# Kernel tuning notes

Hardware: AMD Instinct MI355X
Metric: run time of the kernel (lower is better)

Reference implementation:

```python
import jax, jax.numpy as jnp
import numpy as np

KH = KW = 3
STRIDE = 1
ITERATIONS = 2
EPS = 1e-7


def _squash(s):
    # squash along last axis (capsule dim)
    sn = jnp.sum(s * s, axis=-1, keepdims=True)
    return (sn / (1.0 + sn)) * s / jnp.sqrt(sn + EPS)


def setup_inputs() -> dict:
    key = jax.random.key(0)
    k1, k2 = jax.random.split(key)
    x = jax.random.normal(k1, (4, 14, 14, 32, 8), dtype=jnp.float32)
    # W: [1,1,1,filters_out, caps_per_patch=3*3*32, dims_out=16, dims_in=8], stddev=0.1 init
    W = 0.1 * jax.random.normal(k2, (1, 1, 1, 32, 288, 16, 8), dtype=jnp.float32)
    return {"x": x, "W": W}


def reference(x, W):
    B, H, Wd, Fin, Din = x.shape
    Ho = (H - KH) // STRIDE + 1
    Wo = (Wd - KW) // STRIDE + 1
    # Patch extraction, channel order (kh, kw, Fin) to match tf.image.extract_patches
    patches = jnp.stack(
        [x[:, i:i + Ho * STRIDE:STRIDE, j:j + Wo * STRIDE:STRIDE]
         for i in range(KH) for j in range(KW)],
        axis=3,
    )  # [B,Ho,Wo,KH*KW,Fin,Din]
    patches = patches.reshape(B, Ho, Wo, KH * KW * Fin, Din)  # [B,Ho,Wo,C,Di]

    Wm = W[0, 0, 0]  # [F, C, Do, Di]
    F, C, Do, _ = Wm.shape
    # predictions[b,h,w,f,c,o] = sum_i W[f,c,o,i] * patches[b,h,w,c,i]
    preds = jnp.einsum('fcoi,bhwci->bhwfco', Wm, patches)

    logits = jnp.zeros((B, Ho, Wo, F, C), dtype=preds.dtype)
    outputs = jnp.zeros((B, Ho, Wo, F, Do), dtype=preds.dtype)
    for _ in range(ITERATIONS):
        # agreement = predictions^T @ outputs over the dims_out axis
        agreement = jnp.einsum('bhwfco,bhwfo->bhwfc', preds, outputs)
        logits = logits + agreement
        # NOTE: original code softmaxes over axis=3 (the filters_out axis)
        cc = jax.nn.softmax(logits, axis=3)  # [B,Ho,Wo,F,C]
        centroids = jnp.sum(cc[..., None] * preds, axis=4)  # [B,Ho,Wo,F,Do]
        outputs = _squash(centroids)
    return outputs
```

## Files before the change

### kernel.cpp

```cpp
#include <hip/hip_runtime.h>

#define NB   4
#define H_IN 14
#define W_IN 14
#define FIN  32
#define DI   8
#define F    32
#define C    288
#define DO   16
#define HO   12
#define WO   12
#define NPOS (NB*HO*WO)
#define EPS  1e-7f

#define CH   16
#define CC   (C/CH)
#define GP   2
#define GRID2 ((CH*NPOS/GP)/4)

#define KTOT  (C*DI)
#define KHALF 1152
#define KPADH 1156

#define W2H_BYTES  ((size_t)F*C*DO*DI*2)
#define WH_BYTES   ((size_t)F*C*DO*DI*2)
#define PH_BYTES   ((size_t)NPOS*KTOT*2)
#define PART_BYTES ((size_t)CH*NPOS*F*DO*4)
#define OUT1P_BYTES ((size_t)2*NPOS*F*DO*4)

#define CVT_W   576
#define CVT_PH  648
#define CVT_GRID (CVT_W + CVT_PH)

typedef _Float16 h2 __attribute__((ext_vector_type(2)));
typedef _Float16 h8v __attribute__((ext_vector_type(8)));
typedef float    f4v __attribute__((ext_vector_type(4)));

__device__ __forceinline__ unsigned int pack2(float a, float b) {
    h2 v; v.x = (_Float16)a; v.y = (_Float16)b;
    return __builtin_bit_cast(unsigned int, v);
}

__device__ __forceinline__ float dot8h(const uint4 w, const uint4 v, float acc) {
#if __has_builtin(__builtin_amdgcn_fdot2)
    acc = __builtin_amdgcn_fdot2(__builtin_bit_cast(h2, w.x), __builtin_bit_cast(h2, v.x), acc, false);
    acc = __builtin_amdgcn_fdot2(__builtin_bit_cast(h2, w.y), __builtin_bit_cast(h2, v.y), acc, false);
    acc = __builtin_amdgcn_fdot2(__builtin_bit_cast(h2, w.z), __builtin_bit_cast(h2, v.z), acc, false);
    acc = __builtin_amdgcn_fdot2(__builtin_bit_cast(h2, w.w), __builtin_bit_cast(h2, v.w), acc, false);
#else
    const h2 w0 = __builtin_bit_cast(h2, w.x), v0 = __builtin_bit_cast(h2, v.x);
    const h2 w1 = __builtin_bit_cast(h2, w.y), v1 = __builtin_bit_cast(h2, v.y);
    const h2 w2 = __builtin_bit_cast(h2, w.z), v2 = __builtin_bit_cast(h2, v.z);
    const h2 w3 = __builtin_bit_cast(h2, w.w), v3 = __builtin_bit_cast(h2, v.w);
    acc += (float)w0.x*(float)v0.x + (float)w0.y*(float)v0.y
         + (float)w1.x*(float)v1.x + (float)w1.y*(float)v1.y
         + (float)w2.x*(float)v2.x + (float)w2.y*(float)v2.y
         + (float)w3.x*(float)v3.x + (float)w3.y*(float)v3.y;
#endif
    return acc;
}

__device__ __forceinline__ int xbase_of(int pos) {
    const int b = pos/(HO*WO), rem = pos%(HO*WO), ho = rem/WO, wo = rem%WO;
    return ((b*H_IN + ho)*W_IN + wo)*FIN*DI;
}

__device__ __forceinline__ int coff_of(int c) {
    const int slab = c >> 5, fin = c & 31;
    const int kh = slab/3, kw = slab%3;
    return (kh*W_IN + kw)*FIN*DI + fin*DI;
}

__global__ __launch_bounds__(256) void kernConv(const float* __restrict__ Wt,
                                                const float* __restrict__ x,
                                                unsigned short* __restrict__ W2h,
                                                unsigned short* __restrict__ Wh,
                                                unsigned short* __restrict__ Ph) {
    const int b = blockIdx.x;
    if (b < CVT_W) {
        const int idx = b*256 + threadIdx.x;
        const float* src = Wt + (size_t)idx*8;
        const float4 a = *(const float4*)src;
        const float4 bb = *(const float4*)(src + 4);
        uint4 r;
        r.x = pack2(a.x, a.y);   r.y = pack2(a.z, a.w);
        r.z = pack2(bb.x, bb.y); r.w = pack2(bb.z, bb.w);
        ((uint4*)Wh)[idx] = r;
        const int o = idx & 15;
        const int c = (idx >> 4) % C;
        const int f = idx / (C*DO);
        ((uint4*)W2h)[(size_t)(c*DO + o)*F + f] = r;
    } else {
        const int pc = (b - CVT_W)*256 + threadIdx.x;
        const int pos = pc / C, c = pc % C;
        const float* src = x + xbase_of(pos) + coff_of(c);
        const float4 a = *(const float4*)src;
        const float4 bb = *(const float4*)(src + 4);
        uint4 r;
        r.x = pack2(a.x, a.y);   r.y = pack2(a.z, a.w);
        r.z = pack2(bb.x, bb.y); r.w = pack2(bb.z, bb.w);
        ((uint4*)Ph)[pc] = r;
    }
}

__global__ __launch_bounds__(256) void kernM1(const unsigned short* __restrict__ Ph,
                                              const unsigned short* __restrict__ Wh,
                                              float* __restrict__ out1p)
{
    __shared__ unsigned short As[16][KPADH];

    const int tid  = threadIdx.x;
    const int lane = tid & 63;
    const int wv   = tid >> 6;
    const int ks   = blockIdx.x & 1;
    const int fg   = (blockIdx.x >> 1) & 7;
    const int pt   = blockIdx.x >> 4;
    const int f    = wv*8 + fg;
    const int pos0 = pt*16;
    const int n    = lane & 15, q = lane >> 4;

    #pragma unroll
    for (int r = 0; r < 9; ++r) {
        const int linear = r*256 + tid;
        const int row = linear / 144, col = linear % 144;
        const uint4 v = *(const uint4*)(Ph + (size_t)(pos0 + row)*KTOT + ks*KHALF + col*8);
        *(uint4*)&As[row][col*8] = v;
    }
    __syncthreads();

    const unsigned short* pa = &As[n][q*8];
    const unsigned short* pb = Wh + ((size_t)(f*C + ks*144 + q)*DO + n)*DI;

    f4v acc0 = {0.f,0.f,0.f,0.f}, acc1 = {0.f,0.f,0.f,0.f};
    #pragma unroll 4
    for (int s = 0; s < 36; s += 2) {
        const h8v a0 = *(const h8v*)(pa + s*32);
        const h8v b0 = *(const h8v*)(pb + (size_t)s*4*DO*DI);
        const h8v a1 = *(const h8v*)(pa + (s+1)*32);
        const h8v b1 = *(const h8v*)(pb + (size_t)(s+1)*4*DO*DI);
        acc0 = __builtin_amdgcn_mfma_f32_16x16x32_f16(a0, b0, acc0, 0, 0, 0);
        acc1 = __builtin_amdgcn_mfma_f32_16x16x32_f16(a1, b1, acc1, 0, 0, 0);
    }

    #pragma unroll
    for (int r = 0; r < 4; ++r) {
        out1p[((size_t)ks*NPOS + pos0 + q*4 + r)*512 + f*DO + n] = acc0[r] + acc1[r];
    }
}

__global__ __launch_bounds__(256) void kern2w(const unsigned short* __restrict__ Ph,
                                              const unsigned short* __restrict__ W2h,
                                              const float* __restrict__ out1p,
                                              float* __restrict__ part2)
{
    const int tid  = threadIdx.x;
    const int lane = tid & 63;
    const int wv   = tid >> 6;
    const int f    = lane & 31;
    const int og   = lane >> 5;
    const int o0   = og*8;

    const int ch   = blockIdx.x & (CH-1);
    const int gq   = blockIdx.x >> 4;
    const int grp  = __builtin_amdgcn_readfirstlane(gq*4 + wv);
    const int pos0 = grp*GP;

    const int c0 = ch*CC;
    const uint4* W2h4 = (const uint4*)W2h;

    float u[8][GP];
    #pragma unroll
    for (int p = 0; p < GP; ++p) {
        const float* up0 = out1p + (size_t)(pos0 + p)*512 + f*DO + o0;
        const float* up1 = up0 + (size_t)NPOS*512;
        const float4 a0 = *(const float4*)up0;
        const float4 b0 = *(const float4*)(up0 + 4);
        const float4 a1 = *(const float4*)up1;
        const float4 b1 = *(const float4*)(up1 + 4);
        float ur[8];
        ur[0]=(a0.x+a1.x)*(1.f/32.f); ur[1]=(a0.y+a1.y)*(1.f/32.f);
        ur[2]=(a0.z+a1.z)*(1.f/32.f); ur[3]=(a0.w+a1.w)*(1.f/32.f);
        ur[4]=(b0.x+b1.x)*(1.f/32.f); ur[5]=(b0.y+b1.y)*(1.f/32.f);
        ur[6]=(b0.z+b1.z)*(1.f/32.f); ur[7]=(b0.w+b1.w)*(1.f/32.f);
        float sq = 0.f;
        #pragma unroll
        for (int k = 0; k < 8; ++k) sq += ur[k]*ur[k];
        sq += __shfl_xor(sq, 32);
        const float sc = (sq/(1.f + sq)) * rsqrtf(sq + EPS);
        #pragma unroll
        for (int k = 0; k < 8; ++k) u[k][p] = ur[k]*sc;
    }

    float acc[8][GP];
    #pragma unroll
    for (int k = 0; k < 8; ++k)
        #pragma unroll
        for (int p = 0; p < GP; ++p) acc[k][p] = 0.f;

    #pragma unroll 1
    for (int cl = 0; cl < CC; ++cl) {
        const int c = c0 + cl;

        uint4 xv[GP];
        #pragma unroll
        for (int p = 0; p < GP; ++p)
            xv[p] = *(const uint4*)(Ph + (size_t)(pos0 + p)*KTOT + c*DI);

        float pred[8][GP];
        #pragma unroll
        for (int k = 0; k < 8; ++k) {
            const uint4 w = W2h4[(size_t)(c*DO + o0 + k)*F + f];
            #pragma unroll
            for (int p = 0; p < GP; ++p) pred[k][p] = dot8h(w, xv[p], 0.f);
        }

        #pragma unroll
        for (int p = 0; p < GP; ++p) {
            float ap = 0.f;
            #pragma unroll
            for (int k = 0; k < 8; ++k) ap += pred[k][p]*u[k][p];
            ap += __shfl_xor(ap, 32);

            const float e = __expf(ap);
            float s = e;
            s += __shfl_xor(s, 1);
            s += __shfl_xor(s, 2);
            s += __shfl_xor(s, 4);
            s += __shfl_xor(s, 8);
            s += __shfl_xor(s, 16);
            const float cc = e / s;

            #pragma unroll
            for (int k = 0; k < 8; ++k) acc[k][p] += cc*pred[k][p];
        }
    }

    #pragma unroll
    for (int p = 0; p < GP; ++p) {
        float* dst = part2 + ((size_t)(ch*NPOS + pos0 + p)*F + f)*DO + o0;
        float4 s0, s1;
        s0.x=acc[0][p]; s0.y=acc[1][p]; s0.z=acc[2][p]; s0.w=acc[3][p];
        s1.x=acc[4][p]; s1.y=acc[5][p]; s1.z=acc[6][p]; s1.w=acc[7][p];
        *(float4*)dst = s0;
        *(float4*)(dst + 4) = s1;
    }
}

__global__ __launch_bounds__(256) void kern3(const float* __restrict__ part2,
                                             float* __restrict__ out)
{
    __shared__ float4 red[128];

    const int tid  = threadIdx.x;
    const int pos  = blockIdx.x;
    const int half = tid >> 7;
    const int slot = tid & 127;
    const int f = slot >> 2, q = slot & 3;

    float ax=0.f, ay=0.f, az=0.f, aw=0.f;
    #pragma unroll
    for (int k = 0; k < CH/2; ++k) {
        const int kk = half*(CH/2) + k;
        const float4 v = *(const float4*)(part2 + ((size_t)(kk*NPOS + pos)*F + f)*DO + q*4);
        ax += v.x; ay += v.y; az += v.z; aw += v.w;
    }
    if (half) { float4 r; r.x=ax; r.y=ay; r.z=az; r.w=aw; red[slot] = r; }
    __syncthreads();
    if (!half) {
        const float4 o = red[slot];
        ax += o.x; ay += o.y; az += o.z; aw += o.w;

        float sq = ax*ax + ay*ay + az*az + aw*aw;
        sq += __shfl_xor(sq, 1);
        sq += __shfl_xor(sq, 2);
        const float sc = (sq/(1.f + sq)) * rsqrtf(sq + EPS);

        float4 s; s.x=ax*sc; s.y=ay*sc; s.z=az*sc; s.w=aw*sc;
        *(float4*)(out + ((size_t)pos*F + f)*DO + q*4) = s;
    }
}

__device__ __forceinline__ float dot8(const float4* __restrict__ w,
                                      const float4 p0, const float4 p1) {
    float4 a = w[0], b = w[1];
    return a.x*p0.x + a.y*p0.y + a.z*p0.z + a.w*p0.w
         + b.x*p1.x + b.y*p1.y + b.z*p1.z + b.w*p1.w;
}

__global__ __launch_bounds__(256) void capsule_kernel_f32(
    const float* __restrict__ x, const float* __restrict__ Wt,
    float* __restrict__ out)
{
    __shared__ float patch[C*DI];
    __shared__ float cent[F*DO];
    __shared__ float out1[F*DO];
    __shared__ float agr[F*C];
    __shared__ float scale_s[F];

    const int tid = threadIdx.x;
    const int pos = blockIdx.x;
    const int b   = pos / (HO*WO);
    const int rem = pos % (HO*WO);
    const int ho  = rem / WO;
    const int wo  = rem % WO;

    #pragma unroll
    for (int slab = 0; slab < 9; ++slab) {
        const int kh = slab / 3, kw = slab % 3;
        const float* src = x + (((b*H_IN + ho + kh)*W_IN + (wo + kw))*FIN)*DI;
        patch[slab*256 + tid] = src[tid];
    }
    __syncthreads();

    const float4* pv = (const float4*)patch;

    {
        const int fo0 = tid, fo1 = tid + 256;
        const int f0 = fo0 >> 4, o0 = fo0 & 15;
        const int f1 = fo1 >> 4, o1 = fo1 & 15;
        float acc0 = 0.f, acc1 = 0.f;
        for (int c = 0; c < C; ++c) {
            const float4 p0 = pv[c*2], p1 = pv[c*2+1];
            acc0 += dot8((const float4*)(Wt + ((f0*C + c)*DO + o0)*DI), p0, p1);
            acc1 += dot8((const float4*)(Wt + ((f1*C + c)*DO + o1)*DI), p0, p1);
        }
        cent[fo0] = acc0 * (1.f/32.f);
        cent[fo1] = acc1 * (1.f/32.f);
    }
    __syncthreads();

    if (tid < F) {
        float sn = 0.f;
        #pragma unroll
        for (int o = 0; o < DO; ++o) { float v = cent[tid*DO + o]; sn += v*v; }
        const float sc = (sn/(1.f + sn)) * rsqrtf(sn + EPS);
        #pragma unroll
        for (int o = 0; o < DO; ++o) out1[tid*DO + o] = cent[tid*DO + o] * sc;
    }
    __syncthreads();

    #pragma unroll 1
    for (int r = 0; r < (F*C)/256; ++r) {
        const int pp = tid + 256*r;
        const int f = pp / C, c = pp % C;
        const float4* wrow = (const float4*)(Wt + (f*C + c)*DO*DI);
        const float4 p0 = pv[c*2], p1 = pv[c*2+1];
        float a = 0.f;
        #pragma unroll
        for (int o = 0; o < DO; ++o) a += dot8(wrow + o*2, p0, p1) * out1[f*DO + o];
        agr[pp] = a;
    }
    __syncthreads();

    for (int c = tid; c < C; c += 256) {
        float m = -1e30f;
        #pragma unroll
        for (int f = 0; f < F; ++f) m = fmaxf(m, agr[f*C + c]);
        float s = 0.f;
        #pragma unroll
        for (int f = 0; f < F; ++f) {
            const float e = __expf(agr[f*C + c] - m);
            agr[f*C + c] = e; s += e;
        }
        const float inv = 1.f / s;
        #pragma unroll
        for (int f = 0; f < F; ++f) agr[f*C + c] *= inv;
    }
    __syncthreads();

    {
        const int fo0 = tid, fo1 = tid + 256;
        const int f0 = fo0 >> 4, o0 = fo0 & 15;
        const int f1 = fo1 >> 4, o1 = fo1 & 15;
        float acc0 = 0.f, acc1 = 0.f;
        for (int c = 0; c < C; ++c) {
            const float4 p0 = pv[c*2], p1 = pv[c*2+1];
            acc0 += agr[f0*C + c] * dot8((const float4*)(Wt + ((f0*C + c)*DO + o0)*DI), p0, p1);
            acc1 += agr[f1*C + c] * dot8((const float4*)(Wt + ((f1*C + c)*DO + o1)*DI), p0, p1);
        }
        cent[fo0] = acc0;
        cent[fo1] = acc1;
    }
    __syncthreads();

    if (tid < F) {
        float sn = 0.f;
        #pragma unroll
        for (int o = 0; o < DO; ++o) { float v = cent[tid*DO + o]; sn += v*v; }
        scale_s[tid] = (sn/(1.f + sn)) * rsqrtf(sn + EPS);
    }
    __syncthreads();

    out[pos*(F*DO) + tid]       = cent[tid]       * scale_s[tid >> 4];
    out[pos*(F*DO) + tid + 256] = cent[tid + 256] * scale_s[(tid >> 4) + 16];
}

extern "C" void kernel_launch(void* const* d_in, const int* in_sizes, int n_in,
                              void* d_out, int out_size, void* d_ws, size_t ws_size,
                              hipStream_t stream) {
    const float* x  = (const float*)d_in[0];
    const float* Wt = (const float*)d_in[1];
    float* out = (float*)d_out;

    if (ws_size >= W2H_BYTES + WH_BYTES + PH_BYTES + PART_BYTES + OUT1P_BYTES) {
        char* p = (char*)d_ws;
        unsigned short* W2h = (unsigned short*)p;            p += W2H_BYTES;
        unsigned short* Wh  = (unsigned short*)p;            p += WH_BYTES;
        unsigned short* Ph  = (unsigned short*)p;            p += PH_BYTES;
        float* part = (float*)p;                             p += PART_BYTES;
        float* out1p = (float*)p;

        kernConv<<<CVT_GRID, 256, 0, stream>>>(Wt, x, W2h, Wh, Ph);
        kernM1<<<36*8*2, 256, 0, stream>>>(Ph, Wh, out1p);
        kern2w<<<GRID2, 256, 0, stream>>>(Ph, W2h, out1p, part);
        kern3<<<NPOS, 256, 0, stream>>>(part, out);
    } else {
        capsule_kernel_f32<<<NPOS, 256, 0, stream>>>(x, Wt, out);
    }
}
```

Baseline: 124.3 us.

## Split capsule chunks across two wave halves with LDS reduction in kern2w

Doubles the capsule-axis chunking (CC halves to 9) and uses 512-thread blocks where the upper four waves handle a second chunk and reduce their accumulators into the lower waves through shared memory. The partial buffer stays the same size, since each block still writes one combined partial, so kern3 reads the same amount. This shortens the serial loop per wave and adds parallelism, at the cost of a block-wide barrier, 16KB of LDS per block and possibly lower occupancy from the larger blocks.

```diff
diff --git a/kernel.cpp b/kernel.cpp
--- a/kernel.cpp
+++ b/kernel.cpp
@@ -13,10 +13,11 @@
 #define NPOS (NB*HO*WO)
 #define EPS  1e-7f
 
-#define CH   16
+#define CH   32
+#define CHB  (CH/2)
 #define CC   (C/CH)
 #define GP   2
-#define GRID2 ((CH*NPOS/GP)/4)
+#define GRID2 (CHB*(NPOS/GP)/4)
 
 #define KTOT  (C*DI)
 #define KHALF 1152
@@ -25,7 +26,7 @@
 #define W2H_BYTES  ((size_t)F*C*DO*DI*2)
 #define WH_BYTES   ((size_t)F*C*DO*DI*2)
 #define PH_BYTES   ((size_t)NPOS*KTOT*2)
-#define PART_BYTES ((size_t)CH*NPOS*F*DO*4)
+#define PART_BYTES ((size_t)CHB*NPOS*F*DO*4)
 #define OUT1P_BYTES ((size_t)2*NPOS*F*DO*4)
 
 #define CVT_W   576
@@ -148,24 +149,27 @@
     }
 }
 
-__global__ __launch_bounds__(256) void kern2w(const unsigned short* __restrict__ Ph,
+__global__ __launch_bounds__(512) void kern2w(const unsigned short* __restrict__ Ph,
                                               const unsigned short* __restrict__ W2h,
                                               const float* __restrict__ out1p,
                                               float* __restrict__ part2)
 {
+    __shared__ float red[4][16][64];
+
     const int tid  = threadIdx.x;
     const int lane = tid & 63;
     const int wv   = tid >> 6;
+    const int pr   = wv & 3;
+    const int hi   = wv >> 2;
     const int f    = lane & 31;
     const int og   = lane >> 5;
     const int o0   = og*8;
 
-    const int ch   = blockIdx.x & (CH-1);
+    const int chb  = blockIdx.x & (CHB-1);
     const int gq   = blockIdx.x >> 4;
-    const int grp  = __builtin_amdgcn_readfirstlane(gq*4 + wv);
-    const int pos0 = grp*GP;
-
-    const int c0 = ch*CC;
+    const int pos0 = __builtin_amdgcn_readfirstlane(gq*4 + pr)*GP;
+
+    const int c0 = (2*chb + hi)*CC;
     const uint4* W2h4 = (const uint4*)W2h;
 
     float u[8][GP];
@@ -235,14 +239,30 @@
         }
     }
 
-    #pragma unroll
-    for (int p = 0; p < GP; ++p) {
-        float* dst = part2 + ((size_t)(ch*NPOS + pos0 + p)*F + f)*DO + o0;
-        float4 s0, s1;
-        s0.x=acc[0][p]; s0.y=acc[1][p]; s0.z=acc[2][p]; s0.w=acc[3][p];
-        s1.x=acc[4][p]; s1.y=acc[5][p]; s1.z=acc[6][p]; s1.w=acc[7][p];
-        *(float4*)dst = s0;
-        *(float4*)(dst + 4) = s1;
+    if (hi) {
+        #pragma unroll
+        for (int k = 0; k < 8; ++k)
+            #pragma unroll
+            for (int p = 0; p < GP; ++p)
+                red[pr][k*GP + p][lane] = acc[k][p];
+    }
+    __syncthreads();
+    if (!hi) {
+        #pragma unroll
+        for (int k = 0; k < 8; ++k)
+            #pragma unroll
+            for (int p = 0; p < GP; ++p)
+                acc[k][p] += red[pr][k*GP + p][lane];
+
+        #pragma unroll
+        for (int p = 0; p < GP; ++p) {
+            float* dst = part2 + ((size_t)(chb*NPOS + pos0 + p)*F + f)*DO + o0;
+            float4 s0, s1;
+            s0.x=acc[0][p]; s0.y=acc[1][p]; s0.z=acc[2][p]; s0.w=acc[3][p];
+            s1.x=acc[4][p]; s1.y=acc[5][p]; s1.z=acc[6][p]; s1.w=acc[7][p];
+            *(float4*)dst = s0;
+            *(float4*)(dst + 4) = s1;
+        }
     }
 }
 
@@ -259,8 +279,8 @@
 
     float ax=0.f, ay=0.f, az=0.f, aw=0.f;
     #pragma unroll
-    for (int k = 0; k < CH/2; ++k) {
-        const int kk = half*(CH/2) + k;
+    for (int k = 0; k < CHB/2; ++k) {
+        const int kk = half*(CHB/2) + k;
         const float4 v = *(const float4*)(part2 + ((size_t)(kk*NPOS + pos)*F + f)*DO + q*4);
         ax += v.x; ay += v.y; az += v.z; aw += v.w;
     }
@@ -412,7 +432,7 @@
 
         kernConv<<<CVT_GRID, 256, 0, stream>>>(Wt, x, W2h, Wh, Ph);
         kernM1<<<36*8*2, 256, 0, stream>>>(Ph, Wh, out1p);
-        kern2w<<<GRID2, 256, 0, stream>>>(Ph, W2h, out1p, part);
+        kern2w<<<GRID2, 512, 0, stream>>>(Ph, W2h, out1p, part);
         kern3<<<NPOS, 256, 0, stream>>>(part, out);
     } else {
         capsule_kernel_f32<<<NPOS, 256, 0, stream>>>(x, Wt, out);
```

Result: slower. 132.5 us (+6.7%).
